# Performance work log

Measured on AMD Instinct MI355X. Metric: run time of the kernel, lower is better.

## Reference

```python
import jax, jax.numpy as jnp
import numpy as np

EPS = 1e-8

def rms_norm(x, scale):
    # norm(2,-1)/sqrt(d); x / (rms + eps) * scale
    d = x.shape[-1]
    norm = jnp.sqrt(jnp.sum(x * x, axis=-1, keepdims=True))
    rms = norm / jnp.sqrt(jnp.asarray(d, x.dtype))
    return scale * (x / (rms + EPS))

def setup_inputs() -> dict:
    key = jax.random.key(0)
    B, N, C, FF = 2, 2048, 1024, 4096
    ks = jax.random.split(key, 12)
    s = 0.02
    return {
        "x":  jax.random.normal(ks[0], (B, N, C), jnp.float32),
        "wq": jax.random.normal(ks[1], (C, C), jnp.float32) * s,
        "bq": jnp.zeros((C,), jnp.float32),
        "wk": jax.random.normal(ks[2], (C, C), jnp.float32) * s,
        "bk": jnp.zeros((C,), jnp.float32),
        "wv": jax.random.normal(ks[3], (C, C), jnp.float32) * s,
        "bv": jnp.zeros((C,), jnp.float32),
        "wo": jax.random.normal(ks[4], (C, C), jnp.float32) * s,
        "bo": jnp.zeros((C,), jnp.float32),
        "scale1": jnp.ones((C,), jnp.float32),
        "scale2": jnp.ones((C,), jnp.float32),
        "w1": jax.random.normal(ks[5], (C, FF), jnp.float32) * s,
        "b1": jnp.zeros((FF,), jnp.float32),
        "w2": jax.random.normal(ks[6], (FF, C), jnp.float32) * s,
        "b2": jnp.zeros((C,), jnp.float32),
    }

def reference(x, wq, bq, wk, bk, wv, bv, wo, bo, scale1, scale2, w1, b1, w2, b2):
    B, N, C = x.shape
    H = 16
    D = C // H

    residual = x
    xn = rms_norm(x, scale1)

    def heads(y):  # [B,N,C] -> [B,H,N,D]
        return y.reshape(B, N, H, D).transpose(0, 2, 1, 3)

    q = heads(xn @ wq + bq)
    k = heads(xn @ wk + bk)
    v = heads(xn @ wv + bv)

    # apply_rotary_pos_emb with cos=sin=1: q' = q - roll(q,1,-1), same for k
    q = q - jnp.roll(q, 1, axis=-1)
    k = k - jnp.roll(k, 1, axis=-1)

    # explicit attention (no causal mask in original)
    scores = jnp.einsum('bhnd,bhmd->bhnm', q, k) / jnp.sqrt(jnp.asarray(D, x.dtype))
    probs = jax.nn.softmax(scores, axis=-1)
    attn = jnp.einsum('bhnm,bhmd->bhnd', probs, v)
    attn = attn.transpose(0, 2, 1, 3).reshape(B, N, C)
    attn = attn @ wo + bo

    x = residual + attn
    residual = x
    xn = rms_norm(x, scale2)
    h = jax.nn.gelu(xn @ w1 + b1, approximate=False)  # torch GELU default = exact
    ffn_out = h @ w2 + b2
    return residual + ffn_out
```

## Files before the change

### kernel.cpp

```cpp
#include <hip/hip_runtime.h>
#include <hip/hip_bf16.h>
#include <math.h>

typedef unsigned short u16;
typedef short s16x8 __attribute__((ext_vector_type(8)));
typedef __bf16 bf16x8v __attribute__((ext_vector_type(8)));
typedef float f32x4 __attribute__((ext_vector_type(4)));
typedef unsigned short u16x4 __attribute__((ext_vector_type(4)));

struct Ptr4 { float* p[4]; };
struct TW6 {
    const float* w[6]; u16* o[6]; int mode[6];
    const float *bq, *bk, *bv; float* bqkv;
};

__device__ __forceinline__ u16 f2b(float f) {
    __hip_bfloat16 h = __float2bfloat16(f);
    return __builtin_bit_cast(u16, h);
}

__device__ __forceinline__ float exp2_fast(float x) {
#if __has_builtin(__builtin_amdgcn_exp2f)
    return __builtin_amdgcn_exp2f(x);
#else
    return exp2f(x);
#endif
}

__device__ __forceinline__ f32x4 mfma16(s16x8 a, s16x8 b, f32x4 c) {
    return __builtin_amdgcn_mfma_f32_16x16x32_bf16(
        __builtin_bit_cast(bf16x8v, a), __builtin_bit_cast(bf16x8v, b), c, 0, 0, 0);
}

__device__ __forceinline__ void gl_lds16(const void* g, void* l) {
    typedef const unsigned int __attribute__((address_space(1))) * gp_t;
    typedef unsigned int __attribute__((address_space(3))) * lp_t;
    __builtin_amdgcn_global_load_lds((gp_t)(unsigned long long)g,
                                     (lp_t)(unsigned int)(unsigned long long)l,
                                     16, 0, 0);
}

__device__ __forceinline__ float gelu_fast(float v) {
    float u = 1.5957691216f * (v + 0.044715f * v * v * v);
    return v / (1.f + __expf(-u));
}

#define QSCALE 0.1803368801111244f

__global__ __launch_bounds__(256) void prep_weights(TW6 io) {
    const int z = blockIdx.z, bx = blockIdx.x, by = blockIdx.y;
    const float* W; u16* Wt; int mode = 0, N_, K_, n0, k0;
    if (z < 4) {
        if (bx >= 32) {
            if (z == 0 && bx < 44 && by == 0) {
                const int i = (bx - 32) * 256 + threadIdx.x;
                const int d = i & 1023;
                const int dp = (d & ~63) | ((d + 63) & 63);
                float v;
                if (i < 1024) v = QSCALE * (io.bq[d] - io.bq[dp]);
                else if (i < 2048) v = io.bk[d] - io.bk[dp];
                else v = io.bv[d];
                io.bqkv[i] = v;
            }
            return;
        }
        W = io.w[z]; Wt = io.o[z]; mode = io.mode[z];
        N_ = 1024; K_ = 1024; n0 = bx * 32; k0 = by * 32;
    } else if (z == 4) {
        W = io.w[4]; Wt = io.o[4]; N_ = 4096; K_ = 1024; n0 = bx * 32; k0 = by * 32;
    } else {
        W = io.w[5]; Wt = io.o[5]; N_ = 1024; K_ = 4096; n0 = by * 32; k0 = bx * 32;
    }
    __shared__ u16 tile[32][33];
    const int tx = threadIdx.x & 31, ty = threadIdx.x >> 5;
    const int n = n0 + tx;
    const int np = (n & ~63) | ((n + 63) & 63);
    const float s = (mode == 1) ? QSCALE : 1.f;
#pragma unroll
    for (int i = 0; i < 32; i += 8) {
        const size_t r = (size_t)(k0 + ty + i) * N_;
        float v = W[r + n];
        if (mode) v = (v - W[r + np]) * s;
        tile[ty + i][tx] = f2b(v);
    }
    __syncthreads();
#pragma unroll
    for (int i = 0; i < 32; i += 8)
        Wt[(size_t)(n0 + ty + i) * K_ + k0 + tx] = tile[tx][ty + i];
}

__global__ __launch_bounds__(256) void transpose_v(const u16* __restrict__ qkv,
                                                   u16* __restrict__ vT) {
    __shared__ u16 tile[32][33];
    const int tx = threadIdx.x & 31, ty = threadIdx.x >> 5;
    const int n0 = blockIdx.x * 32, d0 = blockIdx.y * 32, bh = blockIdx.z;
    const int b = bh >> 4, h = bh & 15;
#pragma unroll
    for (int i = 0; i < 32; i += 8)
        tile[ty + i][tx] =
            qkv[(size_t)(b * 2048 + n0 + ty + i) * 3072 + 2048 + h * 64 + d0 + tx];
    __syncthreads();
#pragma unroll
    for (int i = 0; i < 32; i += 8)
        vT[((size_t)bh * 64 + d0 + ty + i) * 2048 + n0 + tx] = tile[tx][ty + i];
}

__global__ __launch_bounds__(256) void rmsnorm_kernel(const float* __restrict__ x,
                                                      const float* __restrict__ scale,
                                                      u16* __restrict__ out) {
    __shared__ float red[4];
    const int t = threadIdx.x, row = blockIdx.x;
    const float4* xr = (const float4*)(x + (size_t)row * 1024);
    float4 v = xr[t];
    float ss = v.x * v.x + v.y * v.y + v.z * v.z + v.w * v.w;
#pragma unroll
    for (int off = 1; off < 64; off <<= 1) ss += __shfl_xor(ss, off);
    if ((t & 63) == 0) red[t >> 6] = ss;
    __syncthreads();
    float tot = red[0] + red[1] + red[2] + red[3];
    float inv = 1.f / (sqrtf(tot * (1.f / 1024.f)) + 1e-8f);
    const float4* sr = (const float4*)scale;
    float4 s = sr[t];
    u16x4 o;
    o[0] = f2b(v.x * inv * s.x);
    o[1] = f2b(v.y * inv * s.y);
    o[2] = f2b(v.z * inv * s.z);
    o[3] = f2b(v.w * inv * s.w);
    ((u16x4*)(out + (size_t)row * 1024))[t] = o;
}

template <int EPI>
__global__ __launch_bounds__(256) void gemm_kernel(const u16* __restrict__ A,
                                                   const u16* __restrict__ Bt,
                                                   const float* __restrict__ bias,
                                                   const float* __restrict__ resid,
                                                   void* __restrict__ outp,
                                                   int M, int N, int K) {
    __shared__ __align__(16) u16 As[128 * 64];
    __shared__ __align__(16) u16 Bs[128 * 64];
    const int t = threadIdx.x, lane = t & 63;
    const int w = t >> 6, wm = (w >> 1) * 64, wn = (w & 1) * 64;
    const int c = lane & 15, qd = lane >> 4;
    const int n0 = blockIdx.x * 128, m0 = blockIdx.y * 128;

    const int srow = t >> 3;
    const int sch8 = ((t & 7) ^ (srow & 7)) * 8;
    const u16* Ag = A + (size_t)(m0 + srow) * K + sch8;
    const u16* Bg = Bt + (size_t)(n0 + srow) * K + sch8;
    const size_t rstride = (size_t)32 * K;

    f32x4 acc[4][4] = {};
    for (int kt = 0; kt < K; kt += 64) {
        __syncthreads();
#pragma unroll
        for (int g = 0; g < 4; g++) {
            gl_lds16(Ag + g * rstride, &As[t * 8 + g * 2048]);
            gl_lds16(Bg + g * rstride, &Bs[t * 8 + g * 2048]);
        }
        Ag += 64;
        Bg += 64;
        __syncthreads();
#pragma unroll
        for (int s = 0; s < 2; s++) {
            s16x8 a[4], b[4];
#pragma unroll
            for (int im = 0; im < 4; im++)
                a[im] = *(const s16x8*)&As[(wm + im * 16 + c) * 64 +
                                           (((s * 4 + qd) ^ (c & 7)) * 8)];
#pragma unroll
            for (int jn = 0; jn < 4; jn++)
                b[jn] = *(const s16x8*)&Bs[(wn + jn * 16 + c) * 64 +
                                           (((s * 4 + qd) ^ (c & 7)) * 8)];
#pragma unroll
            for (int im = 0; im < 4; im++)
#pragma unroll
                for (int jn = 0; jn < 4; jn++)
                    acc[im][jn] = mfma16(a[im], b[jn], acc[im][jn]);
        }
    }

#pragma unroll
    for (int im = 0; im < 4; im++) {
#pragma unroll
        for (int jn = 0; jn < 4; jn++) {
            const int colg = n0 + wn + jn * 16 + c;
            const float bv = bias[colg];
#pragma unroll
            for (int r = 0; r < 4; r++) {
                const int rowg = m0 + wm + im * 16 + qd * 4 + r;
                const size_t off = (size_t)rowg * N + colg;
                float v = acc[im][jn][r] + bv;
                if (EPI == 0) {
                    ((u16*)outp)[off] = f2b(v);
                } else if (EPI == 1) {
                    ((float*)outp)[off] = v + resid[off];
                } else {
                    ((u16*)outp)[off] = f2b(gelu_fast(v));
                }
            }
        }
    }
}

__global__ __launch_bounds__(256) void gemm_splitk(const u16* __restrict__ A,
                                                   const u16* __restrict__ Bt,
                                                   Ptr4 parts,
                                                   int N, int Ktot, int Kc) {
    __shared__ __align__(16) u16 As[128 * 64];
    __shared__ __align__(16) u16 Bs[128 * 64];
    const int t = threadIdx.x, lane = t & 63;
    const int w = t >> 6, wm = (w >> 1) * 64, wn = (w & 1) * 64;
    const int c = lane & 15, qd = lane >> 4;
    const int n0 = blockIdx.x * 128, m0 = blockIdx.y * 128;
    const int z = blockIdx.z;
    float* out = parts.p[z];

    const int srow = t >> 3;
    const int sch8 = ((t & 7) ^ (srow & 7)) * 8;
    const u16* Ag = A + (size_t)(m0 + srow) * Ktot + z * Kc + sch8;
    const u16* Bg = Bt + (size_t)(n0 + srow) * Ktot + z * Kc + sch8;
    const size_t rstride = (size_t)32 * Ktot;

    f32x4 acc[4][4] = {};
    for (int kt = 0; kt < Kc; kt += 64) {
        __syncthreads();
#pragma unroll
        for (int g = 0; g < 4; g++) {
            gl_lds16(Ag + g * rstride, &As[t * 8 + g * 2048]);
            gl_lds16(Bg + g * rstride, &Bs[t * 8 + g * 2048]);
        }
        Ag += 64;
        Bg += 64;
        __syncthreads();
#pragma unroll
        for (int s = 0; s < 2; s++) {
            s16x8 a[4], b[4];
#pragma unroll
            for (int im = 0; im < 4; im++)
                a[im] = *(const s16x8*)&As[(wm + im * 16 + c) * 64 +
                                           (((s * 4 + qd) ^ (c & 7)) * 8)];
#pragma unroll
            for (int jn = 0; jn < 4; jn++)
                b[jn] = *(const s16x8*)&Bs[(wn + jn * 16 + c) * 64 +
                                           (((s * 4 + qd) ^ (c & 7)) * 8)];
#pragma unroll
            for (int im = 0; im < 4; im++)
#pragma unroll
                for (int jn = 0; jn < 4; jn++)
                    acc[im][jn] = mfma16(a[im], b[jn], acc[im][jn]);
        }
    }

#pragma unroll
    for (int im = 0; im < 4; im++)
#pragma unroll
        for (int jn = 0; jn < 4; jn++) {
            const int colg = n0 + wn + jn * 16 + c;
#pragma unroll
            for (int r = 0; r < 4; r++) {
                const int rowg = m0 + wm + im * 16 + qd * 4 + r;
                out[(size_t)rowg * N + colg] = acc[im][jn][r];
            }
        }
}

template <int S, bool NORM>
__global__ __launch_bounds__(256) void reduce_kernel(Ptr4 parts,
                                                     const float* __restrict__ bias,
                                                     const float* __restrict__ resid,
                                                     const float* __restrict__ scale,
                                                     float* __restrict__ yout,
                                                     u16* __restrict__ xnout) {
    __shared__ float red[4];
    const int t = threadIdx.x, row = blockIdx.x;
    const size_t base = (size_t)row * 1024;
    float4 v = ((const float4*)(resid + base))[t];
    float4 bv = ((const float4*)bias)[t];
    v.x += bv.x; v.y += bv.y; v.z += bv.z; v.w += bv.w;
#pragma unroll
    for (int s = 0; s < S; s++) {
        float4 pv = ((const float4*)(parts.p[s] + base))[t];
        v.x += pv.x; v.y += pv.y; v.z += pv.z; v.w += pv.w;
    }
    ((float4*)(yout + base))[t] = v;
    if (NORM) {
        float ss = v.x * v.x + v.y * v.y + v.z * v.z + v.w * v.w;
#pragma unroll
        for (int off = 1; off < 64; off <<= 1) ss += __shfl_xor(ss, off);
        if ((t & 63) == 0) red[t >> 6] = ss;
        __syncthreads();
        float tot = red[0] + red[1] + red[2] + red[3];
        float inv = 1.f / (sqrtf(tot * (1.f / 1024.f)) + 1e-8f);
        float4 s = ((const float4*)scale)[t];
        u16x4 o;
        o[0] = f2b(v.x * inv * s.x);
        o[1] = f2b(v.y * inv * s.y);
        o[2] = f2b(v.z * inv * s.z);
        o[3] = f2b(v.w * inv * s.w);
        ((u16x4*)(xnout + base))[t] = o;
    }
}

__global__ __launch_bounds__(256, 4) void attn_kernel(const u16* __restrict__ qkv,
                                                      const u16* __restrict__ vT,
                                                      u16* __restrict__ attn) {
    __shared__ __align__(16) u16 Ks[2][64 * 64];
    __shared__ __align__(16) u16 Vs[2][64 * 64];
    __shared__ __align__(16) u16 Ps[4 * 16 * 64];

    const int t = threadIdx.x, lane = t & 63, w = t >> 6;
    const int c = lane & 15, qd = lane >> 4;

    const int id = blockIdx.x;
    const int logical = (id & 7) * 128 + (id >> 3);
    const int bh = logical >> 5, qb = logical & 31;
    const int b = bh >> 4, h = bh & 15;
    const int q0 = qb * 64;
    const size_t rowbase = (size_t)b * 2048;

    const u16* kg = qkv + rowbase * 3072 + 1024 + h * 64;
    const u16* vg = vT + (size_t)bh * 64 * 2048;

    const int srow = t >> 3;
    const int sch = (t & 7) ^ (srow & 7);

    const u16* kptr = kg + (size_t)srow * 3072 + sch * 8;
    const u16* vptr = vg + (size_t)srow * 2048 + sch * 8;

    gl_lds16(kptr, &Ks[0][t * 8]);
    gl_lds16(kptr + (size_t)32 * 3072, &Ks[0][2048 + t * 8]);
    gl_lds16(vptr, &Vs[0][t * 8]);
    gl_lds16(vptr + (size_t)32 * 2048, &Vs[0][2048 + t * 8]);

    s16x8 qf[2];
    {
        const u16* qg = qkv + (rowbase + q0 + w * 16) * 3072 + h * 64;
#pragma unroll
        for (int ks = 0; ks < 2; ks++)
            qf[ks] = *(const s16x8*)&qg[(size_t)c * 3072 + ks * 32 + qd * 8];
    }
    __syncthreads();

    const s16x8 ones = {16256, 16256, 16256, 16256, 16256, 16256, 16256, 16256};
    f32x4 lsum = {0.f, 0.f, 0.f, 0.f};
    f32x4 o[4] = {};
    u16* Pw = &Ps[w * 16 * 64];

    for (int it = 0; it < 32; it++) {
        const int buf = it & 1;
        const u16* Kb = Ks[buf];
        const u16* Vb = Vs[buf];

        if (it + 1 < 32) {
            u16* Kn = Ks[buf ^ 1];
            u16* Vn = Vs[buf ^ 1];
            const size_t ko = (size_t)(it + 1) * 64 * 3072;
            const size_t vo = (size_t)(it + 1) * 64;
            gl_lds16(kptr + ko, &Kn[t * 8]);
            gl_lds16(kptr + ko + (size_t)32 * 3072, &Kn[2048 + t * 8]);
            gl_lds16(vptr + vo, &Vn[t * 8]);
            gl_lds16(vptr + vo + (size_t)32 * 2048, &Vn[2048 + t * 8]);
        }

        s16x8 kf[2][4], vf[2][4];
#pragma unroll
        for (int ks = 0; ks < 2; ks++)
#pragma unroll
            for (int j = 0; j < 4; j++) {
                const int rrow = j * 16 + c;
                const int sw = ((ks * 4 + qd) ^ (rrow & 7)) * 8;
                kf[ks][j] = *(const s16x8*)&Kb[rrow * 64 + sw];
                vf[ks][j] = *(const s16x8*)&Vb[rrow * 64 + sw];
            }

        f32x4 sc[4] = {};
        __builtin_amdgcn_s_setprio(1);
#pragma unroll
        for (int ks = 0; ks < 2; ks++)
#pragma unroll
            for (int jn = 0; jn < 4; jn++)
                sc[jn] = mfma16(qf[ks], kf[ks][jn], sc[jn]);
        __builtin_amdgcn_s_setprio(0);

#pragma unroll
        for (int r = 0; r < 4; r++) {
            const int prow = qd * 4 + r;
#pragma unroll
            for (int jn = 0; jn < 4; jn++) {
                float p = exp2_fast(sc[jn][r]);
                Pw[prow * 64 + (((jn * 2 + (c >> 3)) ^ (prow & 7)) * 8) + (c & 7)] =
                    f2b(p);
            }
        }

        __builtin_amdgcn_s_setprio(1);
#pragma unroll
        for (int ks = 0; ks < 2; ks++) {
            s16x8 pf = *(const s16x8*)&Pw[c * 64 + (((ks * 4 + qd) ^ (c & 7)) * 8)];
            lsum = mfma16(pf, ones, lsum);
#pragma unroll
            for (int jd = 0; jd < 4; jd++)
                o[jd] = mfma16(pf, vf[ks][jd], o[jd]);
        }
        __builtin_amdgcn_s_setprio(0);
        __syncthreads();
    }

    const int orow_base = b * 2048 + q0 + w * 16;
#pragma unroll
    for (int r = 0; r < 4; r++) {
        const float inv = 1.f / lsum[r];
        const int grow = orow_base + qd * 4 + r;
#pragma unroll
        for (int jd = 0; jd < 4; jd++)
            attn[(size_t)grow * 1024 + h * 64 + jd * 16 + c] =
                f2b(o[jd][r] * inv);
    }
}

extern "C" void kernel_launch(void* const* d_in, const int* in_sizes, int n_in,
                              void* d_out, int out_size, void* d_ws, size_t ws_size,
                              hipStream_t stream) {
    const float* x = (const float*)d_in[0];
    const float* wq = (const float*)d_in[1];
    const float* bq = (const float*)d_in[2];
    const float* wk = (const float*)d_in[3];
    const float* bk = (const float*)d_in[4];
    const float* wv = (const float*)d_in[5];
    const float* bv = (const float*)d_in[6];
    const float* wo = (const float*)d_in[7];
    const float* bo = (const float*)d_in[8];
    const float* scale1 = (const float*)d_in[9];
    const float* scale2 = (const float*)d_in[10];
    const float* w1 = (const float*)d_in[11];
    const float* b1 = (const float*)d_in[12];
    const float* w2 = (const float*)d_in[13];
    const float* b2 = (const float*)d_in[14];
    float* out = (float*)d_out;

    char* ws = (char*)d_ws;
    size_t off = 0;
    auto alloc = [&](size_t bytes) -> char* {
        char* p = ws + off;
        off += (bytes + 255) & ~(size_t)255;
        return p;
    };
    u16* wqkvT = (u16*)alloc((size_t)3072 * 1024 * 2);
    u16* woT   = (u16*)alloc((size_t)1024 * 1024 * 2);
    u16* w1T   = (u16*)alloc((size_t)4096 * 1024 * 2);
    u16* w2T   = (u16*)alloc((size_t)1024 * 4096 * 2);
    float* bqkv = (float*)alloc(3072 * 4);
    u16* xn    = (u16*)alloc((size_t)4096 * 1024 * 2);
    u16* qkv   = (u16*)alloc((size_t)4096 * 3072 * 2);
    u16* vT    = (u16*)alloc((size_t)32 * 64 * 2048 * 2);
    u16* attnb = (u16*)alloc((size_t)4096 * 1024 * 2);
    float* y1  = (float*)alloc((size_t)4096 * 1024 * 4);
    u16* hbuf  = (u16*)alloc((size_t)4096 * 4096 * 2);

    const size_t SPLIT = (size_t)4096 * 1024;
    Ptr4 po; po.p[0] = (float*)qkv; po.p[1] = (float*)qkv + SPLIT;
    po.p[2] = nullptr; po.p[3] = nullptr;
    Ptr4 pf; pf.p[0] = (float*)xn; pf.p[1] = (float*)xn + SPLIT;
    pf.p[2] = (float*)xn + 2 * SPLIT; pf.p[3] = (float*)wqkvT;

    dim3 blk(256);

    TW6 tw;
    tw.w[0] = wq; tw.o[0] = wqkvT;                          tw.mode[0] = 1;
    tw.w[1] = wk; tw.o[1] = wqkvT + (size_t)1024 * 1024;    tw.mode[1] = 2;
    tw.w[2] = wv; tw.o[2] = wqkvT + (size_t)2048 * 1024;    tw.mode[2] = 0;
    tw.w[3] = wo; tw.o[3] = woT;                            tw.mode[3] = 0;
    tw.w[4] = w1; tw.o[4] = w1T;                            tw.mode[4] = 0;
    tw.w[5] = w2; tw.o[5] = w2T;                            tw.mode[5] = 0;
    tw.bq = bq; tw.bk = bk; tw.bv = bv; tw.bqkv = bqkv;
    prep_weights<<<dim3(128, 32, 6), blk, 0, stream>>>(tw);

    rmsnorm_kernel<<<4096, blk, 0, stream>>>(x, scale1, xn);
    gemm_kernel<0><<<dim3(24, 32), blk, 0, stream>>>(xn, wqkvT, bqkv, nullptr, qkv, 4096, 3072, 1024);
    transpose_v<<<dim3(64, 2, 32), blk, 0, stream>>>(qkv, vT);
    attn_kernel<<<dim3(1024), blk, 0, stream>>>(qkv, vT, attnb);
    gemm_splitk<<<dim3(8, 32, 2), blk, 0, stream>>>(attnb, woT, po, 1024, 1024, 512);
    reduce_kernel<2, true><<<4096, blk, 0, stream>>>(po, bo, x, scale2, y1, xn);
    gemm_kernel<2><<<dim3(32, 32), blk, 0, stream>>>(xn, w1T, b1, nullptr, hbuf, 4096, 4096, 1024);
    gemm_splitk<<<dim3(8, 32, 4), blk, 0, stream>>>(hbuf, w2T, pf, 1024, 4096, 1024);
    reduce_kernel<4, false><<<4096, blk, 0, stream>>>(pf, b2, y1, nullptr, out, nullptr);
}
```

Baseline: 369.3 us.

## Split attention over keys across waves, keep P in registers with transposed MFMA

Rewrites the attention kernel so each wave owns a 16-key slice of every K/V tile for all 64 queries, rather than 16 queries across all keys. Scores are computed transposed (K·Q^T), so the bf16 probabilities feed straight into a 16x16x16 MFMA against V^T without the LDS round trip through Ps. Row sums are accumulated in registers and no longer use the ones-matrix MFMA. The price is a cross-wave reduction of the 64x64 partial outputs through shared memory in three serialized steps, plus more registers, so occupancy drops from 4 to 3 blocks.

```diff
diff --git a/kernel.cpp b/kernel.cpp
--- a/kernel.cpp
+++ b/kernel.cpp
@@ -4,7 +4,9 @@
 
 typedef unsigned short u16;
 typedef short s16x8 __attribute__((ext_vector_type(8)));
+typedef short s16x4 __attribute__((ext_vector_type(4)));
 typedef __bf16 bf16x8v __attribute__((ext_vector_type(8)));
+typedef __bf16 bf16x4v __attribute__((ext_vector_type(4)));
 typedef float f32x4 __attribute__((ext_vector_type(4)));
 typedef unsigned short u16x4 __attribute__((ext_vector_type(4)));
 
@@ -30,6 +32,21 @@
 __device__ __forceinline__ f32x4 mfma16(s16x8 a, s16x8 b, f32x4 c) {
     return __builtin_amdgcn_mfma_f32_16x16x32_bf16(
         __builtin_bit_cast(bf16x8v, a), __builtin_bit_cast(bf16x8v, b), c, 0, 0, 0);
+}
+
+__device__ __forceinline__ f32x4 mfma16k16(s16x4 a, s16x4 b, f32x4 c) {
+#if __has_builtin(__builtin_amdgcn_mfma_f32_16x16x16bf16_1k)
+    return __builtin_amdgcn_mfma_f32_16x16x16bf16_1k(a, b, c, 0, 0, 0);
+#elif __has_builtin(__builtin_amdgcn_mfma_f32_16x16x16_bf16)
+    return __builtin_amdgcn_mfma_f32_16x16x16_bf16(
+        __builtin_bit_cast(bf16x4v, a), __builtin_bit_cast(bf16x4v, b), c, 0, 0, 0);
+#else
+    f32x4 d;
+    asm volatile("v_mfma_f32_16x16x16_bf16 %0, %1, %2, %3"
+                 : "=v"(d)
+                 : "v"(a), "v"(b), "v"(c));
+    return d;
+#endif
 }
 
 __device__ __forceinline__ void gl_lds16(const void* g, void* l) {
@@ -301,15 +318,16 @@
     }
 }
 
-__global__ __launch_bounds__(256, 4) void attn_kernel(const u16* __restrict__ qkv,
+__global__ __launch_bounds__(256, 3) void attn_kernel(const u16* __restrict__ qkv,
                                                       const u16* __restrict__ vT,
                                                       u16* __restrict__ attn) {
-    __shared__ __align__(16) u16 Ks[2][64 * 64];
-    __shared__ __align__(16) u16 Vs[2][64 * 64];
-    __shared__ __align__(16) u16 Ps[4 * 16 * 64];
+    __shared__ __align__(16) char smem[33792];
+    __shared__ float LS[4][64];
+    u16* Ks = (u16*)smem;
+    u16* Vs = (u16*)(smem + 16384);
 
     const int t = threadIdx.x, lane = t & 63, w = t >> 6;
-    const int c = lane & 15, qd = lane >> 4;
+    const int c = lane & 15, g = lane >> 4;
 
     const int id = blockIdx.x;
     const int logical = (id & 7) * 128 + (id >> 3);
@@ -323,37 +341,38 @@
 
     const int srow = t >> 3;
     const int sch = (t & 7) ^ (srow & 7);
-
     const u16* kptr = kg + (size_t)srow * 3072 + sch * 8;
     const u16* vptr = vg + (size_t)srow * 2048 + sch * 8;
 
-    gl_lds16(kptr, &Ks[0][t * 8]);
-    gl_lds16(kptr + (size_t)32 * 3072, &Ks[0][2048 + t * 8]);
-    gl_lds16(vptr, &Vs[0][t * 8]);
-    gl_lds16(vptr + (size_t)32 * 2048, &Vs[0][2048 + t * 8]);
-
-    s16x8 qf[2];
+    gl_lds16(kptr, &Ks[t * 8]);
+    gl_lds16(kptr + (size_t)32 * 3072, &Ks[2048 + t * 8]);
+    gl_lds16(vptr, &Vs[t * 8]);
+    gl_lds16(vptr + (size_t)32 * 2048, &Vs[2048 + t * 8]);
+
+    s16x8 qf[4][2];
     {
-        const u16* qg = qkv + (rowbase + q0 + w * 16) * 3072 + h * 64;
-#pragma unroll
-        for (int ks = 0; ks < 2; ks++)
-            qf[ks] = *(const s16x8*)&qg[(size_t)c * 3072 + ks * 32 + qd * 8];
+        const u16* qg = qkv + (rowbase + q0) * 3072 + h * 64;
+#pragma unroll
+        for (int jn = 0; jn < 4; jn++)
+#pragma unroll
+            for (int ks = 0; ks < 2; ks++)
+                qf[jn][ks] = *(const s16x8*)&qg[(size_t)(jn * 16 + c) * 3072 +
+                                                ks * 32 + g * 8];
     }
     __syncthreads();
 
-    const s16x8 ones = {16256, 16256, 16256, 16256, 16256, 16256, 16256, 16256};
-    f32x4 lsum = {0.f, 0.f, 0.f, 0.f};
-    f32x4 o[4] = {};
-    u16* Pw = &Ps[w * 16 * 64];
+    f32x4 acc[4][4] = {};
+    float ls[4] = {};
+    const int kbase = w * 16;
 
     for (int it = 0; it < 32; it++) {
         const int buf = it & 1;
-        const u16* Kb = Ks[buf];
-        const u16* Vb = Vs[buf];
+        const u16* Kb = Ks + buf * 4096;
+        const u16* Vb = Vs + buf * 4096;
 
         if (it + 1 < 32) {
-            u16* Kn = Ks[buf ^ 1];
-            u16* Vn = Vs[buf ^ 1];
+            u16* Kn = Ks + (buf ^ 1) * 4096;
+            u16* Vn = Vs + (buf ^ 1) * 4096;
             const size_t ko = (size_t)(it + 1) * 64 * 3072;
             const size_t vo = (size_t)(it + 1) * 64;
             gl_lds16(kptr + ko, &Kn[t * 8]);
@@ -362,16 +381,17 @@
             gl_lds16(vptr + vo + (size_t)32 * 2048, &Vn[2048 + t * 8]);
         }
 
-        s16x8 kf[2][4], vf[2][4];
+        s16x8 kf[2];
 #pragma unroll
         for (int ks = 0; ks < 2; ks++)
-#pragma unroll
-            for (int j = 0; j < 4; j++) {
-                const int rrow = j * 16 + c;
-                const int sw = ((ks * 4 + qd) ^ (rrow & 7)) * 8;
-                kf[ks][j] = *(const s16x8*)&Kb[rrow * 64 + sw];
-                vf[ks][j] = *(const s16x8*)&Vb[rrow * 64 + sw];
-            }
+            kf[ks] = *(const s16x8*)&Kb[(kbase + c) * 64 +
+                                        (((ks * 4 + g) ^ (c & 7)) * 8)];
+        s16x4 vf[4];
+#pragma unroll
+        for (int im = 0; im < 4; im++)
+            vf[im] = *(const s16x4*)&Vb[(im * 16 + c) * 64 +
+                                        (((2 * w + (g >> 1)) ^ (c & 7)) * 8) +
+                                        (g & 1) * 4];
 
         f32x4 sc[4] = {};
         __builtin_amdgcn_s_setprio(1);
@@ -379,42 +399,92 @@
         for (int ks = 0; ks < 2; ks++)
 #pragma unroll
             for (int jn = 0; jn < 4; jn++)
-                sc[jn] = mfma16(qf[ks], kf[ks][jn], sc[jn]);
+                sc[jn] = mfma16(kf[ks], qf[jn][ks], sc[jn]);
         __builtin_amdgcn_s_setprio(0);
 
-#pragma unroll
-        for (int r = 0; r < 4; r++) {
-            const int prow = qd * 4 + r;
-#pragma unroll
-            for (int jn = 0; jn < 4; jn++) {
-                float p = exp2_fast(sc[jn][r]);
-                Pw[prow * 64 + (((jn * 2 + (c >> 3)) ^ (prow & 7)) * 8) + (c & 7)] =
-                    f2b(p);
-            }
+        s16x4 pb[4];
+#pragma unroll
+        for (int jn = 0; jn < 4; jn++) {
+            float p0 = exp2_fast(sc[jn][0]);
+            float p1 = exp2_fast(sc[jn][1]);
+            float p2 = exp2_fast(sc[jn][2]);
+            float p3 = exp2_fast(sc[jn][3]);
+            ls[jn] += (p0 + p1) + (p2 + p3);
+            pb[jn][0] = f2b(p0); pb[jn][1] = f2b(p1);
+            pb[jn][2] = f2b(p2); pb[jn][3] = f2b(p3);
         }
 
         __builtin_amdgcn_s_setprio(1);
 #pragma unroll
-        for (int ks = 0; ks < 2; ks++) {
-            s16x8 pf = *(const s16x8*)&Pw[c * 64 + (((ks * 4 + qd) ^ (c & 7)) * 8)];
-            lsum = mfma16(pf, ones, lsum);
-#pragma unroll
-            for (int jd = 0; jd < 4; jd++)
-                o[jd] = mfma16(pf, vf[ks][jd], o[jd]);
-        }
+        for (int im = 0; im < 4; im++)
+#pragma unroll
+            for (int jn = 0; jn < 4; jn++)
+                acc[im][jn] = mfma16k16(vf[im], pb[jn], acc[im][jn]);
         __builtin_amdgcn_s_setprio(0);
         __syncthreads();
     }
 
-    const int orow_base = b * 2048 + q0 + w * 16;
-#pragma unroll
-    for (int r = 0; r < 4; r++) {
-        const float inv = 1.f / lsum[r];
-        const int grow = orow_base + qd * 4 + r;
-#pragma unroll
-        for (int jd = 0; jd < 4; jd++)
-            attn[(size_t)grow * 1024 + h * 64 + jd * 16 + c] =
-                f2b(o[jd][r] * inv);
+#pragma unroll
+    for (int jn = 0; jn < 4; jn++) {
+        float v = ls[jn];
+        v += __shfl_xor(v, 16);
+        v += __shfl_xor(v, 32);
+        ls[jn] = v;
+    }
+    if (lane < 16) {
+#pragma unroll
+        for (int jn = 0; jn < 4; jn++) LS[w][jn * 16 + lane] = ls[jn];
+    }
+
+    float* SC = (float*)smem;
+#pragma unroll
+    for (int src = 3; src >= 1; --src) {
+        __syncthreads();
+        if (w == src) {
+#pragma unroll
+            for (int im = 0; im < 4; im++)
+#pragma unroll
+                for (int jn = 0; jn < 4; jn++)
+#pragma unroll
+                    for (int r = 0; r < 4; r++)
+                        SC[(im * 16 + g * 4 + r) * 66 + jn * 16 + c] =
+                            acc[im][jn][r];
+        }
+        __syncthreads();
+        if (w == src - 1) {
+#pragma unroll
+            for (int im = 0; im < 4; im++)
+#pragma unroll
+                for (int jn = 0; jn < 4; jn++)
+#pragma unroll
+                    for (int r = 0; r < 4; r++)
+                        acc[im][jn][r] +=
+                            SC[(im * 16 + g * 4 + r) * 66 + jn * 16 + c];
+        }
+    }
+    __syncthreads();
+
+    u16* OT = (u16*)smem;
+    if (w == 0) {
+#pragma unroll
+        for (int jn = 0; jn < 4; jn++) {
+            const int q = jn * 16 + c;
+            const float inv = 1.f / (LS[0][q] + LS[1][q] + LS[2][q] + LS[3][q]);
+#pragma unroll
+            for (int im = 0; im < 4; im++)
+#pragma unroll
+                for (int r = 0; r < 4; r++)
+                    OT[q * 72 + im * 16 + g * 4 + r] = f2b(acc[im][jn][r] * inv);
+        }
+    }
+    __syncthreads();
+
+    {
+        const int q = t >> 2, d0 = (t & 3) * 16;
+        const int grow = b * 2048 + q0 + q;
+        u16* dst = attn + (size_t)grow * 1024 + h * 64 + d0;
+        *(s16x8*)dst = *(const s16x8*)&OT[q * 72 + d0];
+        *((s16x8*)dst + 1) = *((const s16x8*)&OT[q * 72 + d0] + 1);
     }
 }
 
```

Measured after the change: 382.7 us. 1.04x slower.
